# Kernel optimization log

Hardware: AMD Instinct MI355X
Metric: run time of the kernel (lower is better)

The kernel has to match this reference:

```python
import jax, jax.numpy as jnp
import numpy as np

NUM_HEADS = 16
NUM_BUCKETS = 32
MAX_DISTANCE = 128


def _rel_bucket(rel):
    # bidirectional T5-style relative position bucketing
    nb = NUM_BUCKETS // 2
    ret = (rel > 0).astype(jnp.int32) * nb
    n = jnp.abs(rel)
    max_exact = nb // 2
    is_small = n < max_exact
    safe = jnp.maximum(n, 1).astype(jnp.float32)
    large = max_exact + (jnp.log(safe / max_exact) / np.log(MAX_DISTANCE / max_exact) * (nb - max_exact)).astype(jnp.int32)
    large = jnp.minimum(large, nb - 1)
    return ret + jnp.where(is_small, n, large)


def setup_inputs() -> dict:
    key = jax.random.key(0)
    ks = jax.random.split(key, 12)
    S, B, E = 1024, 4, 1024
    D = E // NUM_HEADS
    s = 0.02
    return {
        "query": jax.random.normal(ks[0], (S, B, E), jnp.float32),
        "q_w": jax.random.normal(ks[1], (E, E), jnp.float32) * s,
        "q_b": jnp.zeros((E,), jnp.float32),
        "k_w": jax.random.normal(ks[2], (E, E), jnp.float32) * s,
        "k_b": jnp.zeros((E,), jnp.float32),
        "v_w": jax.random.normal(ks[3], (E, E), jnp.float32) * s,
        "v_b": jnp.zeros((E,), jnp.float32),
        "out_w": jax.random.normal(ks[4], (E, E), jnp.float32) * s,
        "out_b": jnp.zeros((E,), jnp.float32),
        "rel_emb": jax.random.normal(ks[5], (NUM_BUCKETS, NUM_HEADS), jnp.float32) * s,
        "grep_w": jax.random.normal(ks[6], (8, D), jnp.float32) * s,
        "grep_b": jnp.zeros((8,), jnp.float32),
        "grep_a": jnp.ones((NUM_HEADS,), jnp.float32),
    }


def reference(query, q_w, q_b, k_w, k_b, v_w, v_b, out_w, out_b, rel_emb, grep_w, grep_b, grep_a):
    S, B, E = query.shape
    H = NUM_HEADS
    D = E // H
    scaling = D ** -0.5

    q = (query @ q_w.T + q_b) * scaling  # scaling applied before gating, as in WavLM
    k = query @ k_w.T + k_b
    v = query @ v_w.T + v_b

    def split(x):  # (S,B,E) -> (B,H,S,D)
        return x.reshape(S, B, H, D).transpose(1, 2, 0, 3)

    q4, k4, v4 = split(q), split(k), split(v)

    attn = jnp.einsum('bhqd,bhkd->bhqk', q4, k4)  # (B,H,S,S)

    pos = jnp.arange(S)
    bucket = _rel_bucket(pos[None, :] - pos[:, None])  # (S,S)
    pbias = rel_emb[bucket].transpose(2, 0, 1)          # (H,S,S)

    # GRU-gated relative position scaling
    g = jnp.einsum('bhsd,ed->bhse', q4, grep_w) + grep_b      # (B,H,S,8)
    g = jax.nn.sigmoid(g.reshape(B, H, S, 2, 4).sum(-1))     # (B,H,S,2)
    gate_a, gate_b = g[..., 0], g[..., 1]
    gate = gate_a * (gate_b * grep_a[None, :, None] - 1.0) + 2.0  # (B,H,S)

    attn = attn + gate[..., None] * pbias[None]
    probs = jax.nn.softmax(attn, axis=-1)
    ctx = jnp.einsum('bhqk,bhkd->bhqd', probs, v4)  # (B,H,S,D)
    out = ctx.transpose(2, 0, 1, 3).reshape(S, B, E) @ out_w.T + out_b
    return out
```

## Files before the change

kernel.cpp:

```cpp
#include <hip/hip_runtime.h>
#include <stdint.h>


typedef short bf16x8 __attribute__((ext_vector_type(8)));
typedef _Float16 f16x8 __attribute__((ext_vector_type(8)));
typedef float f32x4 __attribute__((ext_vector_type(4)));
typedef float f32x16 __attribute__((ext_vector_type(16)));

#define MFMA_BF16(a, b, c) __builtin_amdgcn_mfma_f32_16x16x32_bf16((a), (b), (c), 0, 0, 0)
#define MFMA_F16(a, b, c) __builtin_amdgcn_mfma_f32_16x16x32_f16((a), (b), (c), 0, 0, 0)
#define MFMA32_BF16(a, b, c) __builtin_amdgcn_mfma_f32_32x32x16_bf16((a), (b), (c), 0, 0, 0)

#define LOG2E 1.44269504088896f
#define LN2 0.693147180559945f

__device__ __forceinline__ unsigned short f2bf(float x) {
  union { float f; unsigned u; } v; v.f = x;
  unsigned r = v.u + 0x7fffu + ((v.u >> 16) & 1u);
  return (unsigned short)(r >> 16);
}
__device__ __forceinline__ float bf2f(unsigned short u) {
  union { unsigned u; float f; } v; v.u = ((unsigned)u) << 16;
  return v.f;
}
__device__ __forceinline__ unsigned short f2h(float x) {
  union { _Float16 h; unsigned short u; } v; v.h = (_Float16)x;
  return v.u;
}
__device__ __forceinline__ float u32lo_bf(unsigned u) {
  union { unsigned u; float f; } v; v.u = u << 16;
  return v.f;
}
__device__ __forceinline__ float u32hi_bf(unsigned u) {
  union { unsigned u; float f; } v; v.u = u & 0xffff0000u;
  return v.f;
}

__device__ __forceinline__ void gload_lds16(const void* g, void* l) {
  __builtin_amdgcn_global_load_lds(
      (const __attribute__((address_space(1))) unsigned int*)g,
      (__attribute__((address_space(3))) unsigned int*)l, 16, 0, 0);
}

__device__ __forceinline__ int swz(int row) { return (row ^ (row >> 2)) & 3; }

__global__ __launch_bounds__(256) void prep_kernel(
    const float* __restrict__ query, const float* __restrict__ q_w,
    const float* __restrict__ k_w, const float* __restrict__ v_w,
    const float* __restrict__ out_w, const float* __restrict__ rel_emb,
    unsigned short* __restrict__ q_bf, unsigned short* __restrict__ wq,
    unsigned short* __restrict__ wk, unsigned short* __restrict__ wv,
    unsigned short* __restrict__ ow_h,
    unsigned short* __restrict__ bias_hd) {
  int i = blockIdx.x * 256 + threadIdx.x;
  if (i < 4194304) {
    int e = i & 1023;
    int sb = i >> 10;
    int s = sb >> 2, b = sb & 3;
    q_bf[((size_t)(b * 1024 + s) << 10) | e] = f2bf(query[i]);
  } else if (i < 5242880) {
    int j = i - 4194304;
    wq[j] = f2bf(q_w[j]);
    wk[j] = f2bf(k_w[j]);
    wv[j] = f2bf(v_w[j]);
    ow_h[j] = f2h(out_w[j]);
  } else {
    int idx = i - 5242880;
    if (idx >= 2056) return;
    if (idx >= 2047) {
#pragma unroll
      for (int h = 0; h < 16; ++h) bias_hd[h * 2056 + idx] = 0;
      return;
    }
    int rel = idx - 1023;
    int n = rel < 0 ? -rel : rel;
    int ret = rel > 0 ? 16 : 0;
    int bucket;
    if (n < 8) {
      bucket = ret + n;
    } else {
      int large = 8 + (int)(logf((float)n / 8.0f) / logf(16.0f) * 8.0f);
      if (large > 15) large = 15;
      bucket = ret + large;
    }
#pragma unroll
    for (int h = 0; h < 16; ++h)
      bias_hd[h * 2056 + idx] = f2bf(rel_emb[bucket * 16 + h] * LOG2E);
  }
}

__global__ __launch_bounds__(256, 3) void qkv_gemm_kernel(
    const unsigned short* __restrict__ A, const unsigned short* __restrict__ Wq,
    const unsigned short* __restrict__ Wk, const unsigned short* __restrict__ Wv,
    const float* __restrict__ qb, const float* __restrict__ kb, const float* __restrict__ vb,
    unsigned short* __restrict__ qh,
    unsigned short* __restrict__ kh,
    unsigned short* __restrict__ vT)
{
  __shared__ __align__(16) char smem[32768];
  const int tid = threadIdx.x, lane = tid & 63;
  const int wv_ = tid >> 6;
  const int nt = blockIdx.x;
  const int mt = blockIdx.y;
  const int mat = nt >> 3;
  const unsigned short* W = mat == 0 ? Wq : (mat == 1 ? Wk : Wv);
  const int n0 = (nt & 7) * 128;
  const int m0 = mt * 128;
  const int moff = (wv_ & 1) * 64;
  const int noff = (wv_ >> 1) * 64;

  f32x4 acc[4][4] = {};
  const char* Ab = (const char*)A;
  const char* Wb = (const char*)W;

  int st_row[2], st_g[2];
#pragma unroll
  for (int c = 0; c < 2; ++c) {
    int o = c * 4096 + tid * 16;
    int row = o >> 6, p = (o >> 4) & 3;
    st_row[c] = row;
    st_g[c] = p ^ swz(row);
  }

#define QKV_STAGE(kt, buf)                                                     \
  {                                                                            \
    char* bb = smem + (buf)*16384;                                             \
    _Pragma("unroll") for (int c = 0; c < 2; ++c) {                            \
      int o = c * 4096 + tid * 16;                                             \
      size_t ga = (size_t)(m0 + st_row[c]) * 2048 + (size_t)(kt)*64 + st_g[c] * 16; \
      size_t gb = (size_t)(n0 + st_row[c]) * 2048 + (size_t)(kt)*64 + st_g[c] * 16; \
      gload_lds16(Ab + ga, bb + o);                                            \
      gload_lds16(Wb + gb, bb + 8192 + o);                                     \
    }                                                                          \
  }

  QKV_STAGE(0, 0);
  for (int kt = 0; kt < 32; ++kt) {
    __syncthreads();
    const char* base = smem + (kt & 1) * 16384;
    if (kt < 31) QKV_STAGE(kt + 1, (kt + 1) & 1);

    bf16x8 af[4], bfr[4];
#pragma unroll
    for (int i = 0; i < 4; ++i) {
      int ra = moff + i * 16 + (lane & 15);
      int rb = noff + i * 16 + (lane & 15);
      int q = lane >> 4;
      af[i] = *(const bf16x8*)(base + ra * 64 + (q ^ swz(ra)) * 16);
      bfr[i] = *(const bf16x8*)(base + 8192 + rb * 64 + (q ^ swz(rb)) * 16);
    }
#pragma unroll
    for (int i = 0; i < 4; ++i)
#pragma unroll
      for (int j = 0; j < 4; ++j) acc[i][j] = MFMA_BF16(af[i], bfr[j], acc[i][j]);
  }
#undef QKV_STAGE

  const int bidx = m0 >> 10;
  const int s00 = (m0 & 1023) + moff + ((lane >> 4) << 2);
  const int c0 = n0 + noff + (lane & 15);
  if (mat < 2) {
    const float* barr = mat == 0 ? qb : kb;
    unsigned short* dst = mat == 0 ? qh : kh;
    const float scale = mat == 0 ? (0.125f * LOG2E) : 1.0f;
#pragma unroll
    for (int j = 0; j < 4; ++j) {
      int col = c0 + j * 16;
      int hh = col >> 6, dd = col & 63;
      float bias = barr[col];
#pragma unroll
      for (int i = 0; i < 4; ++i)
#pragma unroll
        for (int r = 0; r < 4; ++r) {
          int s = s00 + i * 16 + r;
          dst[((size_t)(bidx * 16 + hh) * 1024 + s) * 64 + dd] =
              f2bf((acc[i][j][r] + bias) * scale);
        }
    }
  } else {
#pragma unroll
    for (int j = 0; j < 4; ++j) {
      int col = c0 + j * 16;
      int hh = col >> 6, dd = col & 63;
      float bias = vb[col];
#pragma unroll
      for (int i = 0; i < 4; ++i) {
        int s = s00 + i * 16;
        ushort4 pk;
        pk.x = f2bf(acc[i][j][0] + bias);
        pk.y = f2bf(acc[i][j][1] + bias);
        pk.z = f2bf(acc[i][j][2] + bias);
        pk.w = f2bf(acc[i][j][3] + bias);
        *(ushort4*)&vT[((size_t)(bidx * 16 + hh) * 64 + dd) * 1024 + s] = pk;
      }
    }
  }
}

__global__ __launch_bounds__(256) void gate_kernel(const unsigned short* __restrict__ qh,
                                                   const float* __restrict__ grep_w,
                                                   const float* __restrict__ grep_b,
                                                   const float* __restrict__ grep_a,
                                                   float* __restrict__ gate) {
  __shared__ float gw[512];
  __shared__ float gbb[8];
  __shared__ float gaa[16];
  int tid = threadIdx.x;
  for (int i = tid; i < 512; i += 256) gw[i] = grep_w[i];
  if (tid < 8) gbb[tid] = grep_b[tid];
  if (tid < 16) gaa[tid] = grep_a[tid];
  __syncthreads();
  int idx = blockIdx.x * 256 + tid;
  int h = (idx >> 10) & 15;
  const unsigned short* qrow = qh + (size_t)idx * 64;
  float a[8] = {0.f, 0.f, 0.f, 0.f, 0.f, 0.f, 0.f, 0.f};
#pragma unroll
  for (int c = 0; c < 8; ++c) {
    bf16x8 v = *(const bf16x8*)(qrow + c * 8);
#pragma unroll
    for (int jj = 0; jj < 8; ++jj) {
      float qv = bf2f((unsigned short)v[jj]);
      int d = c * 8 + jj;
#pragma unroll
      for (int e = 0; e < 8; ++e) a[e] += qv * gw[e * 64 + d];
    }
  }
  float sa = (a[0] + a[1] + a[2] + a[3]) * LN2 + gbb[0] + gbb[1] + gbb[2] + gbb[3];
  float sb = (a[4] + a[5] + a[6] + a[7]) * LN2 + gbb[4] + gbb[5] + gbb[6] + gbb[7];
  float siga = 1.f / (1.f + __expf(-sa));
  float sigb = 1.f / (1.f + __expf(-sb));
  gate[idx] = siga * (sigb * gaa[h] - 1.f) + 2.f;
}

__global__ __launch_bounds__(256, 2) void attn_kernel(
    const unsigned short* __restrict__ qh, const unsigned short* __restrict__ kh,
    const unsigned short* __restrict__ vT, const float* __restrict__ gate,
    const unsigned short* __restrict__ bias_hd, unsigned short* __restrict__ ctx) {
  __shared__ __align__(16) char smem[53760];
  const int tid = threadIdx.x, lane = tid & 63, w = tid >> 6;
  const int bh = blockIdx.x;
  const int h = bh & 15;
  const int qs0 = blockIdx.y * 128;
  const int q31 = lane & 31, hb = lane >> 5, q7 = q31 & 7;
  const int sq = qs0 + w * 32 + q31;

  unsigned short* bc0 = (unsigned short*)(smem + 49152);
  unsigned short* bc1 = (unsigned short*)(smem + 51456);
  {
    const unsigned short* gb = bias_hd + h * 2056 + (896 - qs0);
    for (int i = tid; i < 1152; i += 256) {
      bc0[i] = gb[i];
      bc1[i] = gb[i + 1];
    }
  }

  const char* kbase = (const char*)(kh + (size_t)bh * 65536);
  const char* vbase = (const char*)(vT + (size_t)bh * 65536);

  const int o1 = tid * 16, o2 = o1 + 4096;
  const int r1 = o1 >> 7, r2 = o2 >> 7;
  const int g1 = ((o1 >> 4) & 7) ^ (r1 & 7);
  const int g2 = ((o2 >> 4) & 7) ^ (r2 & 7);
  const size_t k1 = (size_t)r1 * 128 + g1 * 16, k2 = (size_t)r2 * 128 + g2 * 16;
  const size_t v1 = (size_t)r1 * 2048 + g1 * 16, v2 = (size_t)r2 * 2048 + g2 * 16;

  gload_lds16(kbase + k1, smem + o1);
  gload_lds16(kbase + k2, smem + o2);
  gload_lds16(vbase + v1, smem + 16384 + o1);
  gload_lds16(vbase + v2, smem + 16384 + o2);

  const unsigned short* qrow = qh + ((size_t)bh * 1024 + sq) * 64 + hb * 8;
  bf16x8 qf[4];
#pragma unroll
  for (int dc = 0; dc < 4; ++dc) qf[dc] = *(const bf16x8*)(qrow + dc * 16);

  const float gate_lane = gate[bh * 1024 + sq];

  const int par = (127 - w * 32 - q31) & 1;
  const unsigned int* bp = (const unsigned int*)(par ? bc1 : bc0);
  const int bbase0 = (qs0 + 127 - sq - par) >> 1;

  char* psrow = smem + 32768 + (w * 32 + q31) * 128;

  float l_run = 0.f;
  f32x16 accO0 = {}, accO1 = {};

  for (int kc = 0; kc < 16; ++kc) {
    __syncthreads();
    const char* Kc = smem + (kc & 1) * 8192;
    const char* Vc = smem + 16384 + (kc & 1) * 8192;
    if (kc < 15) {
      int nb = (kc + 1) & 1;
      gload_lds16(kbase + (size_t)(kc + 1) * 8192 + k1, smem + nb * 8192 + o1);
      gload_lds16(kbase + (size_t)(kc + 1) * 8192 + k2, smem + nb * 8192 + o2);
      gload_lds16(vbase + (size_t)(kc + 1) * 128 + v1, smem + 16384 + nb * 8192 + o1);
      gload_lds16(vbase + (size_t)(kc + 1) * 128 + v2, smem + 16384 + nb * 8192 + o2);
    }

    f32x16 sacA = {}, sacB = {};
#pragma unroll
    for (int ks = 0; ks < 4; ++ks) {
      int ch = ((ks * 2 + hb) ^ q7) << 4;
      bf16x8 k0 = *(const bf16x8*)(Kc + q31 * 128 + ch);
      bf16x8 kk1 = *(const bf16x8*)(Kc + (32 + q31) * 128 + ch);
      sacA = MFMA32_BF16(k0, qf[ks], sacA);
      sacB = MFMA32_BF16(kk1, qf[ks], sacB);
    }

    float ps = 0.f;
#pragma unroll
    for (int kt = 0; kt < 2; ++kt) {
#pragma unroll
      for (int rg = 0; rg < 4; ++rg) {
        int runoff = kt * 32 + rg * 8 + hb * 4;
        int idx = bbase0 + ((kc * 64 + runoff) >> 1);
        unsigned int u0 = bp[idx], u1 = bp[idx + 1];
        float s0v = (kt ? sacB : sacA)[rg * 4 + 0];
        float s1v = (kt ? sacB : sacA)[rg * 4 + 1];
        float s2v = (kt ? sacB : sacA)[rg * 4 + 2];
        float s3v = (kt ? sacB : sacA)[rg * 4 + 3];
        float p0 = __builtin_exp2f(__builtin_fmaf(gate_lane, u32lo_bf(u0), s0v));
        float p1 = __builtin_exp2f(__builtin_fmaf(gate_lane, u32hi_bf(u0), s1v));
        float p2 = __builtin_exp2f(__builtin_fmaf(gate_lane, u32lo_bf(u1), s2v));
        float p3 = __builtin_exp2f(__builtin_fmaf(gate_lane, u32hi_bf(u1), s3v));
        ps += (p0 + p1) + (p2 + p3);
        ushort4 pk;
        pk.x = f2bf(p0); pk.y = f2bf(p1); pk.z = f2bf(p2); pk.w = f2bf(p3);
        int c = kt * 4 + rg;
        *(ushort4*)(psrow + ((c ^ q7) << 4) + hb * 8) = pk;
      }
    }
    l_run += ps;

#pragma unroll
    for (int ks = 0; ks < 4; ++ks) {
      int cc = (ks * 2 + hb) ^ q7;
      bf16x8 pb = *(const bf16x8*)(psrow + (cc << 4));
      int ch = cc << 4;
      bf16x8 v0f = *(const bf16x8*)(Vc + q31 * 128 + ch);
      bf16x8 v1f = *(const bf16x8*)(Vc + (32 + q31) * 128 + ch);
      accO0 = MFMA32_BF16(v0f, pb, accO0);
      accO1 = MFMA32_BF16(v1f, pb, accO1);
    }
  }

  l_run += __shfl_xor(l_run, 32, 64);
  const float inv = 1.0f / l_run;

  __syncthreads();
  float* Ot = (float*)smem;
  {
    float* ow = Ot + (w * 32 + q31) * 68;
#pragma unroll
    for (int rr = 0; rr < 16; ++rr) {
      int d = (rr & 3) + 8 * (rr >> 2) + 4 * hb;
      ow[d] = accO0[rr] * inv;
      ow[32 + d] = accO1[rr] * inv;
    }
  }
  __syncthreads();
  {
    int row = tid >> 1, dg = tid & 1;
    int s = qs0 + row;
    const float* src = Ot + row * 68 + dg * 32;
    unsigned short hbuf[32];
#pragma unroll
    for (int j = 0; j < 32; ++j) hbuf[j] = f2h(src[j]);
    size_t base = (size_t)(s * 4 + (bh >> 4)) * 1024 + h * 64 + dg * 32;
#pragma unroll
    for (int qd = 0; qd < 4; ++qd)
      *(uint4*)(ctx + base + qd * 8) = *(const uint4*)(hbuf + qd * 8);
  }
}

__global__ __launch_bounds__(256, 3) void outproj_kernel(
    const unsigned short* __restrict__ Af,
    const unsigned short* __restrict__ Bf,
    const float* __restrict__ ob, float* __restrict__ out) {
  __shared__ __align__(16) char smem[24576];
  const int tid = threadIdx.x, lane = tid & 63, wv_ = tid >> 6;
  const int q15 = lane & 15, quad = lane >> 4;
  const int n0 = blockIdx.x * 128;
  const int m0 = blockIdx.y * 64;
  const int moff = (wv_ & 1) * 32;
  const int noff = (wv_ >> 1) * 64;

  const int oa = tid * 16;
  const int ra_ = oa >> 6;
  const int ga_ = (((oa >> 4) & 3) ^ swz(ra_)) << 4;
  int rb_[2], gb_[2], obo_[2];
#pragma unroll
  for (int c = 0; c < 2; ++c) {
    int ob2 = c * 4096 + tid * 16;
    obo_[c] = ob2;
    rb_[c] = ob2 >> 6;
    gb_[c] = (((ob2 >> 4) & 3) ^ swz(rb_[c])) << 4;
  }

#define OP_STAGE(kt, buf)                                                        \
  {                                                                              \
    char* bb = smem + (buf)*12288;                                               \
    size_t ga = (size_t)(m0 + ra_) * 2048 + (size_t)(kt)*64 + ga_;               \
    gload_lds16((const char*)Af + ga, bb + oa);                                  \
    _Pragma("unroll") for (int c = 0; c < 2; ++c) {                              \
      size_t gb = (size_t)(n0 + rb_[c]) * 2048 + (size_t)(kt)*64 + gb_[c];       \
      gload_lds16((const char*)Bf + gb, bb + 4096 + obo_[c]);                    \
    }                                                                            \
  }

  f32x4 acc[2][4] = {};
  OP_STAGE(0, 0);
  for (int kt = 0; kt < 32; ++kt) {
    __syncthreads();
    const char* base = smem + (kt & 1) * 12288;
    if (kt < 31) OP_STAGE(kt + 1, (kt + 1) & 1);

    f16x8 ah[2], bhf[4];
#pragma unroll
    for (int i = 0; i < 2; ++i) {
      int ra = moff + i * 16 + q15;
      ah[i] = *(const f16x8*)(base + ra * 64 + ((quad ^ swz(ra)) << 4));
    }
#pragma unroll
    for (int j = 0; j < 4; ++j) {
      int rb = noff + j * 16 + q15;
      bhf[j] = *(const f16x8*)(base + 4096 + rb * 64 + ((quad ^ swz(rb)) << 4));
    }
#pragma unroll
    for (int i = 0; i < 2; ++i)
#pragma unroll
      for (int j = 0; j < 4; ++j) acc[i][j] = MFMA_F16(ah[i], bhf[j], acc[i][j]);
  }
#undef OP_STAGE

  const int rr0 = m0 + moff + (quad << 2);
  const int c0 = n0 + noff + q15;
#pragma unroll
  for (int j = 0; j < 4; ++j) {
    int col = c0 + j * 16;
    float bias = ob[col];
#pragma unroll
    for (int i = 0; i < 2; ++i)
#pragma unroll
      for (int r = 0; r < 4; ++r)
        out[(size_t)(rr0 + i * 16 + r) * 1024 + col] = acc[i][j][r] + bias;
  }
}

extern "C" void kernel_launch(void* const* d_in, const int* in_sizes, int n_in,
                              void* d_out, int out_size, void* d_ws, size_t ws_size,
                              hipStream_t stream) {
  const float* query = (const float*)d_in[0];
  const float* q_w = (const float*)d_in[1];
  const float* q_b = (const float*)d_in[2];
  const float* k_w = (const float*)d_in[3];
  const float* k_b = (const float*)d_in[4];
  const float* v_w = (const float*)d_in[5];
  const float* v_b = (const float*)d_in[6];
  const float* out_w = (const float*)d_in[7];
  const float* out_b = (const float*)d_in[8];
  const float* rel_emb = (const float*)d_in[9];
  const float* grep_w = (const float*)d_in[10];
  const float* grep_b = (const float*)d_in[11];
  const float* grep_a = (const float*)d_in[12];
  float* out = (float*)d_out;

  const size_t MB = 1u << 20;
  char* ws = (char*)d_ws;
  unsigned short* q_bf = (unsigned short*)(ws);
  unsigned short* wq_bf = (unsigned short*)(ws + 8 * MB);
  unsigned short* wk_bf = (unsigned short*)(ws + 10 * MB);
  unsigned short* wv_bf = (unsigned short*)(ws + 12 * MB);
  unsigned short* ow_h = (unsigned short*)(ws + 14 * MB);
  unsigned short* qhp = (unsigned short*)(ws + 16 * MB);
  unsigned short* khp = (unsigned short*)(ws + 24 * MB);
  unsigned short* vTp = (unsigned short*)(ws + 32 * MB);
  unsigned short* ctxp = (unsigned short*)(ws + 40 * MB);
  float* gatep = (float*)(ws + 48 * MB);
  unsigned short* biasp = (unsigned short*)(ws + 48 * MB + 256 * 1024);

  prep_kernel<<<20489, 256, 0, stream>>>(query, q_w, k_w, v_w, out_w, rel_emb, q_bf, wq_bf,
                                         wk_bf, wv_bf, ow_h, biasp);
  qkv_gemm_kernel<<<dim3(24, 32), 256, 0, stream>>>(q_bf, wq_bf, wk_bf, wv_bf, q_b, k_b, v_b,
                                                    qhp, khp, vTp);
  gate_kernel<<<256, 256, 0, stream>>>(qhp, grep_w, grep_b, grep_a, gatep);
  attn_kernel<<<dim3(64, 8), 256, 0, stream>>>(qhp, khp, vTp, gatep, biasp, ctxp);
  outproj_kernel<<<dim3(8, 64), 256, 0, stream>>>(ctxp, ow_h, out_b, out);
}
```

Measured before the change: 200.0 us.

## Split each key chunk across wave pairs in attention kernel and combine partials

Doubles the attention block to 512 threads so two waves share each 32-query tile, each handling half of every 64-key chunk for QK, exp and PV. Partial output accumulators and row sums are combined through LDS at the end before normalisation. This aims to raise wave-level parallelism and hide latency, at the cost of larger LDS use per block, an extra reduction pass with barriers, and possibly lower block residency.

Result: faster. 193.1 us (-3.4%).

```diff
diff --git a/kernel.cpp b/kernel.cpp
--- a/kernel.cpp
+++ b/kernel.cpp
@@ -232,23 +232,24 @@
   gate[idx] = siga * (sigb * gaa[h] - 1.f) + 2.f;
 }
 
-__global__ __launch_bounds__(256, 2) void attn_kernel(
+__global__ __launch_bounds__(512, 4) void attn_kernel(
     const unsigned short* __restrict__ qh, const unsigned short* __restrict__ kh,
     const unsigned short* __restrict__ vT, const float* __restrict__ gate,
     const unsigned short* __restrict__ bias_hd, unsigned short* __restrict__ ctx) {
-  __shared__ __align__(16) char smem[53760];
+  __shared__ __align__(16) char smem[70144];
   const int tid = threadIdx.x, lane = tid & 63, w = tid >> 6;
+  const int qt = w >> 1, khalf = w & 1;
   const int bh = blockIdx.x;
   const int h = bh & 15;
   const int qs0 = blockIdx.y * 128;
   const int q31 = lane & 31, hb = lane >> 5, q7 = q31 & 7;
-  const int sq = qs0 + w * 32 + q31;
-
-  unsigned short* bc0 = (unsigned short*)(smem + 49152);
-  unsigned short* bc1 = (unsigned short*)(smem + 51456);
+  const int sq = qs0 + qt * 32 + q31;
+
+  unsigned short* bc0 = (unsigned short*)(smem + 65536);
+  unsigned short* bc1 = (unsigned short*)(smem + 67840);
   {
     const unsigned short* gb = bias_hd + h * 2056 + (896 - qs0);
-    for (int i = tid; i < 1152; i += 256) {
+    for (int i = tid; i < 1152; i += 512) {
       bc0[i] = gb[i];
       bc1[i] = gb[i + 1];
     }
@@ -257,17 +258,14 @@
   const char* kbase = (const char*)(kh + (size_t)bh * 65536);
   const char* vbase = (const char*)(vT + (size_t)bh * 65536);
 
-  const int o1 = tid * 16, o2 = o1 + 4096;
-  const int r1 = o1 >> 7, r2 = o2 >> 7;
-  const int g1 = ((o1 >> 4) & 7) ^ (r1 & 7);
-  const int g2 = ((o2 >> 4) & 7) ^ (r2 & 7);
-  const size_t k1 = (size_t)r1 * 128 + g1 * 16, k2 = (size_t)r2 * 128 + g2 * 16;
-  const size_t v1 = (size_t)r1 * 2048 + g1 * 16, v2 = (size_t)r2 * 2048 + g2 * 16;
-
-  gload_lds16(kbase + k1, smem + o1);
-  gload_lds16(kbase + k2, smem + o2);
-  gload_lds16(vbase + v1, smem + 16384 + o1);
-  gload_lds16(vbase + v2, smem + 16384 + o2);
+  const int o = tid * 16;
+  const int srow = o >> 7;
+  const int sg = ((o >> 4) & 7) ^ (srow & 7);
+  const size_t koff = (size_t)srow * 128 + sg * 16;
+  const size_t voff = (size_t)srow * 2048 + sg * 16;
+
+  gload_lds16(kbase + koff, smem + o);
+  gload_lds16(vbase + voff, smem + 16384 + o);
 
   const unsigned short* qrow = qh + ((size_t)bh * 1024 + sq) * 64 + hb * 8;
   bf16x8 qf[4];
@@ -276,7 +274,7 @@
 
   const float gate_lane = gate[bh * 1024 + sq];
 
-  const int par = (127 - w * 32 - q31) & 1;
+  const int par = (127 - q31) & 1;
   const unsigned int* bp = (const unsigned int*)(par ? bc1 : bc0);
   const int bbase0 = (qs0 + 127 - sq - par) >> 1;
 
@@ -291,85 +289,80 @@
     const char* Vc = smem + 16384 + (kc & 1) * 8192;
     if (kc < 15) {
       int nb = (kc + 1) & 1;
-      gload_lds16(kbase + (size_t)(kc + 1) * 8192 + k1, smem + nb * 8192 + o1);
-      gload_lds16(kbase + (size_t)(kc + 1) * 8192 + k2, smem + nb * 8192 + o2);
-      gload_lds16(vbase + (size_t)(kc + 1) * 128 + v1, smem + 16384 + nb * 8192 + o1);
-      gload_lds16(vbase + (size_t)(kc + 1) * 128 + v2, smem + 16384 + nb * 8192 + o2);
-    }
-
-    f32x16 sacA = {}, sacB = {};
+      gload_lds16(kbase + (size_t)(kc + 1) * 8192 + koff, smem + nb * 8192 + o);
+      gload_lds16(vbase + (size_t)(kc + 1) * 128 + voff, smem + 16384 + nb * 8192 + o);
+    }
+
+    f32x16 sac = {};
+    const char* Krow = Kc + (khalf * 32 + q31) * 128;
 #pragma unroll
     for (int ks = 0; ks < 4; ++ks) {
-      int ch = ((ks * 2 + hb) ^ q7) << 4;
-      bf16x8 k0 = *(const bf16x8*)(Kc + q31 * 128 + ch);
-      bf16x8 kk1 = *(const bf16x8*)(Kc + (32 + q31) * 128 + ch);
-      sacA = MFMA32_BF16(k0, qf[ks], sacA);
-      sacB = MFMA32_BF16(kk1, qf[ks], sacB);
+      bf16x8 kf = *(const bf16x8*)(Krow + (((ks * 2 + hb) ^ q7) << 4));
+      sac = MFMA32_BF16(kf, qf[ks], sac);
     }
 
     float ps = 0.f;
 #pragma unroll
-    for (int kt = 0; kt < 2; ++kt) {
-#pragma unroll
-      for (int rg = 0; rg < 4; ++rg) {
-        int runoff = kt * 32 + rg * 8 + hb * 4;
-        int idx = bbase0 + ((kc * 64 + runoff) >> 1);
-        unsigned int u0 = bp[idx], u1 = bp[idx + 1];
-        float s0v = (kt ? sacB : sacA)[rg * 4 + 0];
-        float s1v = (kt ? sacB : sacA)[rg * 4 + 1];
-        float s2v = (kt ? sacB : sacA)[rg * 4 + 2];
-        float s3v = (kt ? sacB : sacA)[rg * 4 + 3];
-        float p0 = __builtin_exp2f(__builtin_fmaf(gate_lane, u32lo_bf(u0), s0v));
-        float p1 = __builtin_exp2f(__builtin_fmaf(gate_lane, u32hi_bf(u0), s1v));
-        float p2 = __builtin_exp2f(__builtin_fmaf(gate_lane, u32lo_bf(u1), s2v));
-        float p3 = __builtin_exp2f(__builtin_fmaf(gate_lane, u32hi_bf(u1), s3v));
-        ps += (p0 + p1) + (p2 + p3);
-        ushort4 pk;
-        pk.x = f2bf(p0); pk.y = f2bf(p1); pk.z = f2bf(p2); pk.w = f2bf(p3);
-        int c = kt * 4 + rg;
-        *(ushort4*)(psrow + ((c ^ q7) << 4) + hb * 8) = pk;
-      }
+    for (int rg = 0; rg < 4; ++rg) {
+      int idx = bbase0 + ((kc * 64 + khalf * 32 + rg * 8 + hb * 4) >> 1);
+      unsigned u0 = bp[idx], u1 = bp[idx + 1];
+      float p0 = __builtin_exp2f(__builtin_fmaf(gate_lane, u32lo_bf(u0), sac[rg * 4 + 0]));
+      float p1 = __builtin_exp2f(__builtin_fmaf(gate_lane, u32hi_bf(u0), sac[rg * 4 + 1]));
+      float p2 = __builtin_exp2f(__builtin_fmaf(gate_lane, u32lo_bf(u1), sac[rg * 4 + 2]));
+      float p3 = __builtin_exp2f(__builtin_fmaf(gate_lane, u32hi_bf(u1), sac[rg * 4 + 3]));
+      ps += (p0 + p1) + (p2 + p3);
+      ushort4 pk;
+      pk.x = f2bf(p0); pk.y = f2bf(p1); pk.z = f2bf(p2); pk.w = f2bf(p3);
+      *(ushort4*)(psrow + ((rg ^ q7) << 4) + hb * 8) = pk;
     }
     l_run += ps;
 
 #pragma unroll
-    for (int ks = 0; ks < 4; ++ks) {
-      int cc = (ks * 2 + hb) ^ q7;
-      bf16x8 pb = *(const bf16x8*)(psrow + (cc << 4));
-      int ch = cc << 4;
-      bf16x8 v0f = *(const bf16x8*)(Vc + q31 * 128 + ch);
-      bf16x8 v1f = *(const bf16x8*)(Vc + (32 + q31) * 128 + ch);
+    for (int mf = 0; mf < 2; ++mf) {
+      bf16x8 pb = *(const bf16x8*)(psrow + (((mf * 2 + hb) ^ q7) << 4));
+      int vch = ((khalf * 4 + mf * 2 + hb) ^ q7) << 4;
+      bf16x8 v0f = *(const bf16x8*)(Vc + q31 * 128 + vch);
+      bf16x8 v1f = *(const bf16x8*)(Vc + (32 + q31) * 128 + vch);
       accO0 = MFMA32_BF16(v0f, pb, accO0);
       accO1 = MFMA32_BF16(v1f, pb, accO1);
     }
   }
 
   l_run += __shfl_xor(l_run, 32, 64);
-  const float inv = 1.0f / l_run;
 
   __syncthreads();
   float* Ot = (float*)smem;
-  {
-    float* ow = Ot + (w * 32 + q31) * 68;
+  float* ow = Ot + (qt * 32 + q31) * 68;
+  if (khalf == 0) {
 #pragma unroll
     for (int rr = 0; rr < 16; ++rr) {
       int d = (rr & 3) + 8 * (rr >> 2) + 4 * hb;
-      ow[d] = accO0[rr] * inv;
-      ow[32 + d] = accO1[rr] * inv;
+      ow[d] = accO0[rr];
+      ow[32 + d] = accO1[rr];
+    }
+    if (hb == 0) ow[64] = l_run;
+  }
+  __syncthreads();
+  if (khalf == 1) {
+    float inv = 1.0f / (ow[64] + l_run);
+#pragma unroll
+    for (int rr = 0; rr < 16; ++rr) {
+      int d = (rr & 3) + 8 * (rr >> 2) + 4 * hb;
+      ow[d] = (ow[d] + accO0[rr]) * inv;
+      ow[32 + d] = (ow[32 + d] + accO1[rr]) * inv;
     }
   }
   __syncthreads();
   {
-    int row = tid >> 1, dg = tid & 1;
+    int row = tid >> 2, dg = tid & 3;
     int s = qs0 + row;
-    const float* src = Ot + row * 68 + dg * 32;
-    unsigned short hbuf[32];
-#pragma unroll
-    for (int j = 0; j < 32; ++j) hbuf[j] = f2h(src[j]);
-    size_t base = (size_t)(s * 4 + (bh >> 4)) * 1024 + h * 64 + dg * 32;
-#pragma unroll
-    for (int qd = 0; qd < 4; ++qd)
-      *(uint4*)(ctx + base + qd * 8) = *(const uint4*)(hbuf + qd * 8);
+    const float* src = Ot + row * 68 + dg * 16;
+    unsigned short hbuf[16];
+#pragma unroll
+    for (int j = 0; j < 16; ++j) hbuf[j] = f2h(src[j]);
+    size_t base = (size_t)(s * 4 + (bh >> 4)) * 1024 + h * 64 + dg * 16;
+    *(uint4*)(ctx + base) = *(const uint4*)(hbuf);
+    *(uint4*)(ctx + base + 8) = *(const uint4*)(hbuf + 8);
   }
 }
 
@@ -484,6 +477,6 @@
   qkv_gemm_kernel<<<dim3(24, 32), 256, 0, stream>>>(q_bf, wq_bf, wk_bf, wv_bf, q_b, k_b, v_b,
                                                     qhp, khp, vTp);
   gate_kernel<<<256, 256, 0, stream>>>(qhp, grep_w, grep_b, grep_a, gatep);
-  attn_kernel<<<dim3(64, 8), 256, 0, stream>>>(qhp, khp, vTp, gatep, biasp, ctxp);
+  attn_kernel<<<dim3(64, 8), 512, 0, stream>>>(qhp, khp, vTp, gatep, biasp, ctxp);
   outproj_kernel<<<dim3(8, 64), 256, 0, stream>>>(ctxp, ow_h, out_b, out);
 }
```
